# Optimization experiments

Measured on AMD Instinct MI355X. Metric: run time of the kernel, lower is better.

Reference implementation:

```python
import jax, jax.numpy as jnp
import numpy as np

B, H, S, D = 2, 16, 2048, 128


def setup_inputs() -> dict:
    key = jax.random.key(0)
    kq, kk, kv, km = jax.random.split(key, 4)
    Q = jax.random.normal(kq, (B, H, S, D), dtype=jnp.float32)
    K = jax.random.normal(kk, (B, H, S, D), dtype=jnp.float32)
    V = jax.random.normal(kv, (B, H, S, D), dtype=jnp.float32)
    mask = jax.random.randint(km, (B, 1, S, S), 0, 2, dtype=jnp.int32)
    scale = jnp.float32(1.0 / np.sqrt(D))
    return {"Q": Q, "K": K, "V": V, "mask": mask, "scale": scale}


def reference(Q, K, V, mask, scale):
    # attention scores: [B, H, Sq, Sk]
    attention = jnp.einsum('bhqd,bhkd->bhqk', Q, K) * scale
    NEG_BIG = jnp.float32(-1e9)
    attention = jnp.where(mask == 0, NEG_BIG, attention)
    attention = jax.nn.softmax(attention, axis=-1)
    # context: [B, H, Sq, Dv]
    context = jnp.einsum('bhqk,bhkd->bhqd', attention, V)
    return (context, attention)
```

## Files before the change

kernel.cpp:

```cpp
#include <hip/hip_runtime.h>

#define Bb 2
#define Hh 16
#define Ss 2048
#define Dd 128
#define NWrd (Ss / 64)
#define NBLK (Bb * Hh * (Ss / 64))

typedef _Float16 half_t;
typedef __attribute__((ext_vector_type(4))) float floatx4;
typedef __attribute__((ext_vector_type(8))) _Float16 halfx8;
typedef unsigned long long u64;

__global__ __launch_bounds__(256) void cvt_qk_kernel(
    const float* __restrict__ Q, const float* __restrict__ K,
    const float* __restrict__ scale_p,
    half_t* __restrict__ Qh, half_t* __restrict__ Kh) {
  const float s = scale_p[0];
  size_t i = ((size_t)blockIdx.x * 256 + threadIdx.x) * 8;
  floatx4 a0 = *(const floatx4*)(Q + i);
  floatx4 a1 = *(const floatx4*)(Q + i + 4);
  halfx8 hq = {(half_t)(a0.x * s), (half_t)(a0.y * s), (half_t)(a0.z * s),
               (half_t)(a0.w * s), (half_t)(a1.x * s), (half_t)(a1.y * s),
               (half_t)(a1.z * s), (half_t)(a1.w * s)};
  *(halfx8*)(Qh + i) = hq;
  floatx4 b0 = *(const floatx4*)(K + i);
  floatx4 b1 = *(const floatx4*)(K + i + 4);
  halfx8 hk = {(half_t)b0.x, (half_t)b0.y, (half_t)b0.z, (half_t)b0.w,
               (half_t)b1.x, (half_t)b1.y, (half_t)b1.z, (half_t)b1.w};
  *(halfx8*)(Kh + i) = hk;
}

__global__ __launch_bounds__(256) void vt_kernel(const float* __restrict__ V,
                                                 half_t* __restrict__ Vt) {
  __shared__ __align__(16) half_t t[64 * 72];
  const int bh = blockIdx.z;
  const int k0 = blockIdx.x * 64;
  const int d0 = blockIdx.y * 64;
  const int tid = threadIdx.x;
  const float* src = V + ((size_t)bh * Ss + k0) * Dd + d0;
  for (int idx = tid; idx < 64 * 16; idx += 256) {
    int r = idx >> 4;
    int c4 = (idx & 15) << 2;
    floatx4 v = *(const floatx4*)(src + (size_t)r * Dd + c4);
    t[(c4 + 0) * 72 + r] = (half_t)v.x;
    t[(c4 + 1) * 72 + r] = (half_t)v.y;
    t[(c4 + 2) * 72 + r] = (half_t)v.z;
    t[(c4 + 3) * 72 + r] = (half_t)v.w;
  }
  __syncthreads();
  half_t* dst = Vt + ((size_t)bh * Dd + d0) * Ss + k0;
  for (int idx = tid; idx < 64 * 8; idx += 256) {
    int r = idx >> 3;
    int c8 = (idx & 7) << 3;
    *(halfx8*)(dst + (size_t)r * Ss + c8) = *(const halfx8*)&t[r * 72 + c8];
  }
}

__global__ __launch_bounds__(256) void mask_pack_kernel(
    const int* __restrict__ mask, u64* __restrict__ mb) {
  size_t w = (size_t)blockIdx.x * 4 + (threadIdx.x >> 6);
  int lane = threadIdx.x & 63;
  int m = mask[w * 64 + lane];
  u64 bal = __ballot(m != 0);
  if (lane == 0) mb[w] = bal;
}

__global__ __launch_bounds__(256, 4) void attn_kernel(
    const half_t* __restrict__ Qh, const half_t* __restrict__ Kh,
    const u64* __restrict__ Mb, const half_t* __restrict__ Vt,
    float* __restrict__ ctx_out, float* __restrict__ attn_out) {
  __shared__ __align__(16) half_t Ks[64 * 136];
  __shared__ __align__(16) half_t Ps[4 * 16 * 72];

  const int tid = threadIdx.x;
  const int wave = tid >> 6;
  const int lane = tid & 63;
  const int quad = lane >> 4;
  const int l16 = lane & 15;

  const int wg = blockIdx.x + 32 * (blockIdx.y + Hh * blockIdx.z);
  const int v = (wg & 7) * (NBLK / 8) + (wg >> 3);
  const int q0 = (v & 31) * 64;
  const int bh = v >> 5;
  const int bidx = bh >> 4;

  const half_t* Qg = Qh + ((size_t)bh * Ss + q0) * Dd;
  const half_t* Kg = Kh + (size_t)bh * Ss * Dd;
  const half_t* Vtg = Vt + (size_t)bh * Dd * Ss;
  const u64* Mg = Mb + ((size_t)bidx * Ss + q0) * NWrd;

  const int arow = 16 * wave + l16;
  halfx8 qa[4];
#pragma unroll
  for (int ks = 0; ks < 4; ++ks)
    qa[ks] = *(const halfx8*)(Qg + (size_t)arow * Dd + ks * 32 + quad * 8);

  const int lrow = 16 * wave + quad * 4;
  const int qrow = q0 + lrow;
  const u64* Mrow = Mg + (size_t)lrow * NWrd;
  float lacc[4] = {0.f, 0.f, 0.f, 0.f};

  const int s_r = tid >> 4;
  const int s_c = (tid & 15) << 3;

  halfx8 kpre[4];
#pragma unroll
  for (int it = 0; it < 4; ++it)
    kpre[it] = *(const halfx8*)(Kg + (size_t)(s_r + it * 16) * Dd + s_c);

  for (int kt = 0; kt < NWrd; ++kt) {
    const int k0 = kt * 64;
    __syncthreads();
#pragma unroll
    for (int it = 0; it < 4; ++it)
      *(halfx8*)&Ks[(s_r + it * 16) * 136 + s_c] = kpre[it];
    if (kt + 1 < NWrd) {
#pragma unroll
      for (int it = 0; it < 4; ++it)
        kpre[it] = *(const halfx8*)(Kg + (size_t)(k0 + 64 + s_r + it * 16) * Dd + s_c);
    }
    u64 mw[4];
#pragma unroll
    for (int r = 0; r < 4; ++r) mw[r] = Mrow[(size_t)r * NWrd + kt];
    __syncthreads();
#pragma unroll
    for (int nt = 0; nt < 4; ++nt) {
      floatx4 acc = {0.f, 0.f, 0.f, 0.f};
#pragma unroll
      for (int ks = 0; ks < 4; ++ks) {
        halfx8 bf = *(const halfx8*)&Ks[(nt * 16 + l16) * 136 + ks * 32 + quad * 8];
        acc = __builtin_amdgcn_mfma_f32_16x16x32_f16(qa[ks], bf, acc, 0, 0, 0);
      }
      const int sh = nt * 16 + l16;
#pragma unroll
      for (int r = 0; r < 4; ++r) {
        float e = ((mw[r] >> sh) & 1) ? __expf(acc[r]) : 0.0f;
        lacc[r] += e;
      }
    }
  }
  float inv[4];
#pragma unroll
  for (int r = 0; r < 4; ++r) {
    float s = lacc[r];
    s += __shfl_xor(s, 1);
    s += __shfl_xor(s, 2);
    s += __shfl_xor(s, 4);
    s += __shfl_xor(s, 8);
    inv[r] = 1.0f / s;
  }

  floatx4 cacc[8];
#pragma unroll
  for (int i = 0; i < 8; ++i) cacc[i] = (floatx4){0.f, 0.f, 0.f, 0.f};
  float* attn_row = attn_out + (size_t)bh * Ss * Ss + (size_t)qrow * Ss;

#pragma unroll
  for (int it = 0; it < 4; ++it)
    kpre[it] = *(const halfx8*)(Kg + (size_t)(s_r + it * 16) * Dd + s_c);

  for (int kt = 0; kt < NWrd; ++kt) {
    const int k0 = kt * 64;
    __syncthreads();
#pragma unroll
    for (int it = 0; it < 4; ++it)
      *(halfx8*)&Ks[(s_r + it * 16) * 136 + s_c] = kpre[it];
    if (kt + 1 < NWrd) {
#pragma unroll
      for (int it = 0; it < 4; ++it)
        kpre[it] = *(const halfx8*)(Kg + (size_t)(k0 + 64 + s_r + it * 16) * Dd + s_c);
    }
    u64 mw[4];
#pragma unroll
    for (int r = 0; r < 4; ++r) mw[r] = Mrow[(size_t)r * NWrd + kt];
    __syncthreads();
#pragma unroll
    for (int nt = 0; nt < 4; ++nt) {
      floatx4 acc = {0.f, 0.f, 0.f, 0.f};
#pragma unroll
      for (int ks = 0; ks < 4; ++ks) {
        halfx8 bf = *(const halfx8*)&Ks[(nt * 16 + l16) * 136 + ks * 32 + quad * 8];
        acc = __builtin_amdgcn_mfma_f32_16x16x32_f16(qa[ks], bf, acc, 0, 0, 0);
      }
      const int sh = nt * 16 + l16;
#pragma unroll
      for (int r = 0; r < 4; ++r) {
        float p = ((mw[r] >> sh) & 1) ? __expf(acc[r]) * inv[r] : 0.0f;
        __builtin_nontemporal_store(p, &attn_row[(size_t)r * Ss + k0 + sh]);
        Ps[wave * (16 * 72) + (quad * 4 + r) * 72 + sh] = (half_t)p;
      }
    }
    halfx8 pa0 = *(const halfx8*)&Ps[wave * (16 * 72) + l16 * 72 + quad * 8];
    halfx8 pa1 = *(const halfx8*)&Ps[wave * (16 * 72) + l16 * 72 + 32 + quad * 8];
#pragma unroll
    for (int nt2 = 0; nt2 < 8; ++nt2) {
      const half_t* vrow = Vtg + (size_t)(nt2 * 16 + l16) * Ss + k0 + quad * 8;
      halfx8 bv0 = *(const halfx8*)(vrow);
      cacc[nt2] = __builtin_amdgcn_mfma_f32_16x16x32_f16(pa0, bv0, cacc[nt2], 0, 0, 0);
      halfx8 bv1 = *(const halfx8*)(vrow + 32);
      cacc[nt2] = __builtin_amdgcn_mfma_f32_16x16x32_f16(pa1, bv1, cacc[nt2], 0, 0, 0);
    }
  }

  float* ctx = ctx_out + (size_t)bh * Ss * Dd;
#pragma unroll
  for (int nt2 = 0; nt2 < 8; ++nt2) {
#pragma unroll
    for (int r = 0; r < 4; ++r) {
      ctx[(size_t)(qrow + r) * Dd + nt2 * 16 + l16] = cacc[nt2][r];
    }
  }
}

extern "C" void kernel_launch(void* const* d_in, const int* in_sizes, int n_in,
                              void* d_out, int out_size, void* d_ws, size_t ws_size,
                              hipStream_t stream) {
  const float* Q = (const float*)d_in[0];
  const float* K = (const float*)d_in[1];
  const float* V = (const float*)d_in[2];
  const int* mask = (const int*)d_in[3];
  const float* scale = (const float*)d_in[4];
  float* ctx = (float*)d_out;
  float* attn = (float*)d_out + (size_t)Bb * Hh * Ss * Dd;

  const size_t nqk = (size_t)Bb * Hh * Ss * Dd;
  half_t* Qh = (half_t*)d_ws;
  half_t* Kh = Qh + nqk;
  half_t* Vt = Kh + nqk;
  u64* Mbits = (u64*)(Vt + nqk);

  cvt_qk_kernel<<<nqk / (256 * 8), 256, 0, stream>>>(Q, K, scale, Qh, Kh);
  dim3 gt(Ss / 64, Dd / 64, Bb * Hh);
  vt_kernel<<<gt, 256, 0, stream>>>(V, Vt);
  mask_pack_kernel<<<((size_t)Bb * Ss * NWrd) / 4, 256, 0, stream>>>(mask, Mbits);
  dim3 gm(Ss / 64, Hh, Bb);
  attn_kernel<<<gm, 256, 0, stream>>>(Qh, Kh, Mbits, Vt, ctx, attn);
}
```

Before: 887.2 us.

## Read K fragments directly from global memory and fold log2e into Q scale

Removes the shared-memory K tile, its register prefetch and both block-wide barriers per key tile. Each wave now loads its K MFMA operands straight from global memory and relies on the cache for reuse across the four waves. Q is prescaled by log2(e), so the softmax uses exp2f instead of __expf. An explicit lgkmcnt wait is added before reading back the per-wave P tile, which would otherwise rely on the barrier that was removed. The risk is more global/L2 traffic and latency for K, since the four waves now fetch the same K rows redundantly.

```diff
diff --git a/kernel.cpp b/kernel.cpp
--- a/kernel.cpp
+++ b/kernel.cpp
@@ -16,7 +16,7 @@
     const float* __restrict__ Q, const float* __restrict__ K,
     const float* __restrict__ scale_p,
     half_t* __restrict__ Qh, half_t* __restrict__ Kh) {
-  const float s = scale_p[0];
+  const float s = scale_p[0] * 1.4426950408889634f;
   size_t i = ((size_t)blockIdx.x * 256 + threadIdx.x) * 8;
   floatx4 a0 = *(const floatx4*)(Q + i);
   floatx4 a1 = *(const floatx4*)(Q + i + 4);
@@ -70,7 +70,6 @@
     const half_t* __restrict__ Qh, const half_t* __restrict__ Kh,
     const u64* __restrict__ Mb, const half_t* __restrict__ Vt,
     float* __restrict__ ctx_out, float* __restrict__ attn_out) {
-  __shared__ __align__(16) half_t Ks[64 * 136];
   __shared__ __align__(16) half_t Ps[4 * 16 * 72];
 
   const int tid = threadIdx.x;
@@ -101,41 +100,24 @@
   const u64* Mrow = Mg + (size_t)lrow * NWrd;
   float lacc[4] = {0.f, 0.f, 0.f, 0.f};
 
-  const int s_r = tid >> 4;
-  const int s_c = (tid & 15) << 3;
-
-  halfx8 kpre[4];
-#pragma unroll
-  for (int it = 0; it < 4; ++it)
-    kpre[it] = *(const halfx8*)(Kg + (size_t)(s_r + it * 16) * Dd + s_c);
-
   for (int kt = 0; kt < NWrd; ++kt) {
     const int k0 = kt * 64;
-    __syncthreads();
-#pragma unroll
-    for (int it = 0; it < 4; ++it)
-      *(halfx8*)&Ks[(s_r + it * 16) * 136 + s_c] = kpre[it];
-    if (kt + 1 < NWrd) {
-#pragma unroll
-      for (int it = 0; it < 4; ++it)
-        kpre[it] = *(const halfx8*)(Kg + (size_t)(k0 + 64 + s_r + it * 16) * Dd + s_c);
-    }
     u64 mw[4];
 #pragma unroll
     for (int r = 0; r < 4; ++r) mw[r] = Mrow[(size_t)r * NWrd + kt];
-    __syncthreads();
 #pragma unroll
     for (int nt = 0; nt < 4; ++nt) {
+      const half_t* krow = Kg + (size_t)(k0 + nt * 16 + l16) * Dd + quad * 8;
       floatx4 acc = {0.f, 0.f, 0.f, 0.f};
 #pragma unroll
       for (int ks = 0; ks < 4; ++ks) {
-        halfx8 bf = *(const halfx8*)&Ks[(nt * 16 + l16) * 136 + ks * 32 + quad * 8];
+        halfx8 bf = *(const halfx8*)(krow + ks * 32);
         acc = __builtin_amdgcn_mfma_f32_16x16x32_f16(qa[ks], bf, acc, 0, 0, 0);
       }
       const int sh = nt * 16 + l16;
 #pragma unroll
       for (int r = 0; r < 4; ++r) {
-        float e = ((mw[r] >> sh) & 1) ? __expf(acc[r]) : 0.0f;
+        float e = ((mw[r] >> sh) & 1) ? exp2f(acc[r]) : 0.0f;
         lacc[r] += e;
       }
     }
@@ -156,41 +138,29 @@
   for (int i = 0; i < 8; ++i) cacc[i] = (floatx4){0.f, 0.f, 0.f, 0.f};
   float* attn_row = attn_out + (size_t)bh * Ss * Ss + (size_t)qrow * Ss;
 
-#pragma unroll
-  for (int it = 0; it < 4; ++it)
-    kpre[it] = *(const halfx8*)(Kg + (size_t)(s_r + it * 16) * Dd + s_c);
-
   for (int kt = 0; kt < NWrd; ++kt) {
     const int k0 = kt * 64;
-    __syncthreads();
-#pragma unroll
-    for (int it = 0; it < 4; ++it)
-      *(halfx8*)&Ks[(s_r + it * 16) * 136 + s_c] = kpre[it];
-    if (kt + 1 < NWrd) {
-#pragma unroll
-      for (int it = 0; it < 4; ++it)
-        kpre[it] = *(const halfx8*)(Kg + (size_t)(k0 + 64 + s_r + it * 16) * Dd + s_c);
-    }
     u64 mw[4];
 #pragma unroll
     for (int r = 0; r < 4; ++r) mw[r] = Mrow[(size_t)r * NWrd + kt];
-    __syncthreads();
 #pragma unroll
     for (int nt = 0; nt < 4; ++nt) {
+      const half_t* krow = Kg + (size_t)(k0 + nt * 16 + l16) * Dd + quad * 8;
       floatx4 acc = {0.f, 0.f, 0.f, 0.f};
 #pragma unroll
       for (int ks = 0; ks < 4; ++ks) {
-        halfx8 bf = *(const halfx8*)&Ks[(nt * 16 + l16) * 136 + ks * 32 + quad * 8];
+        halfx8 bf = *(const halfx8*)(krow + ks * 32);
         acc = __builtin_amdgcn_mfma_f32_16x16x32_f16(qa[ks], bf, acc, 0, 0, 0);
       }
       const int sh = nt * 16 + l16;
 #pragma unroll
       for (int r = 0; r < 4; ++r) {
-        float p = ((mw[r] >> sh) & 1) ? __expf(acc[r]) * inv[r] : 0.0f;
+        float p = ((mw[r] >> sh) & 1) ? exp2f(acc[r]) * inv[r] : 0.0f;
         __builtin_nontemporal_store(p, &attn_row[(size_t)r * Ss + k0 + sh]);
         Ps[wave * (16 * 72) + (quad * 4 + r) * 72 + sh] = (half_t)p;
       }
     }
+    asm volatile("s_waitcnt lgkmcnt(0)" ::: "memory");
     halfx8 pa0 = *(const halfx8*)&Ps[wave * (16 * 72) + l16 * 72 + quad * 8];
     halfx8 pa1 = *(const halfx8*)&Ps[wave * (16 * 72) + l16 * 72 + 32 + quad * 8];
 #pragma unroll
```

After: 1.292 ms. 1.46x slower.

## Cache unnormalized fp16 probabilities in workspace instead of recomputing QK^T

Applied to the files above, without the earlier changes.

The first pass now writes the unnormalized exp scores as fp16 to a global workspace. The second pass reads them back, normalizes, stores the attention matrix, and multiplies by V staged through shared memory, so the second QK^T matmul is gone. The log2e factor is folded into the Q scale so exp2f can replace __expf. This swaps recompute for extra global traffic (an fp16 S×S write and read), and the old two-pass kernel is kept as a fallback when the workspace is too small.

```diff
diff --git a/kernel.cpp b/kernel.cpp
--- a/kernel.cpp
+++ b/kernel.cpp
@@ -16,7 +16,7 @@
     const float* __restrict__ Q, const float* __restrict__ K,
     const float* __restrict__ scale_p,
     half_t* __restrict__ Qh, half_t* __restrict__ Kh) {
-  const float s = scale_p[0];
+  const float s = scale_p[0] * 1.4426950408889634f;
   size_t i = ((size_t)blockIdx.x * 256 + threadIdx.x) * 8;
   floatx4 a0 = *(const floatx4*)(Q + i);
   floatx4 a1 = *(const floatx4*)(Q + i + 4);
@@ -66,12 +66,16 @@
   if (lane == 0) mb[w] = bal;
 }
 
-__global__ __launch_bounds__(256, 4) void attn_kernel(
+__global__ __launch_bounds__(256, 4) void attn_fused(
     const half_t* __restrict__ Qh, const half_t* __restrict__ Kh,
     const u64* __restrict__ Mb, const half_t* __restrict__ Vt,
-    float* __restrict__ ctx_out, float* __restrict__ attn_out) {
-  __shared__ __align__(16) half_t Ks[64 * 136];
-  __shared__ __align__(16) half_t Ps[4 * 16 * 72];
+    half_t* __restrict__ Pw, float* __restrict__ ctx_out,
+    float* __restrict__ attn_out) {
+  __shared__ __align__(16) half_t smem[64 * 136 + 4 * 16 * 72];
+  __shared__ float invs[64];
+  half_t* Ks = smem;
+  half_t* Ps = smem + 64 * 136;
+  half_t* Vts = smem;
 
   const int tid = threadIdx.x;
   const int wave = tid >> 6;
@@ -89,6 +93,7 @@
   const half_t* Kg = Kh + (size_t)bh * Ss * Dd;
   const half_t* Vtg = Vt + (size_t)bh * Dd * Ss;
   const u64* Mg = Mb + ((size_t)bidx * Ss + q0) * NWrd;
+  half_t* Pwg = Pw + ((size_t)bh * Ss + q0) * Ss;
 
   const int arow = 16 * wave + l16;
   halfx8 qa[4];
@@ -101,6 +106,8 @@
   const u64* Mrow = Mg + (size_t)lrow * NWrd;
   float lacc[4] = {0.f, 0.f, 0.f, 0.f};
 
+  half_t* Pl = Pwg + (size_t)arow * Ss + quad * 8;
+
   const int s_r = tid >> 4;
   const int s_c = (tid & 15) << 3;
 
@@ -135,11 +142,18 @@
       const int sh = nt * 16 + l16;
 #pragma unroll
       for (int r = 0; r < 4; ++r) {
-        float e = ((mw[r] >> sh) & 1) ? __expf(acc[r]) : 0.0f;
+        float e = ((mw[r] >> sh) & 1) ? exp2f(acc[r]) : 0.0f;
         lacc[r] += e;
-      }
-    }
-  }
+        Ps[wave * (16 * 72) + (quad * 4 + r) * 72 + sh] = (half_t)e;
+      }
+    }
+    asm volatile("s_waitcnt lgkmcnt(0)" ::: "memory");
+    halfx8 pa0 = *(const halfx8*)&Ps[wave * (16 * 72) + l16 * 72 + quad * 8];
+    halfx8 pa1 = *(const halfx8*)&Ps[wave * (16 * 72) + l16 * 72 + 32 + quad * 8];
+    *(halfx8*)(Pl + k0) = pa0;
+    *(halfx8*)(Pl + k0 + 32) = pa1;
+  }
+
   float inv[4];
 #pragma unroll
   for (int r = 0; r < 4; ++r) {
@@ -150,12 +164,117 @@
     s += __shfl_xor(s, 8);
     inv[r] = 1.0f / s;
   }
+#pragma unroll
+  for (int r = 0; r < 4; ++r) invs[wave * 16 + quad * 4 + r] = inv[r];
+  __syncthreads();
+  const float invf = invs[wave * 16 + l16];
 
   floatx4 cacc[8];
 #pragma unroll
   for (int i = 0; i < 8; ++i) cacc[i] = (floatx4){0.f, 0.f, 0.f, 0.f};
-  float* attn_row = attn_out + (size_t)bh * Ss * Ss + (size_t)qrow * Ss;
-
+  float* arow_p = attn_out + ((size_t)bh * Ss + q0 + arow) * Ss + quad * 8;
+
+  const int v_r = tid >> 3;
+  const int v_c = (tid & 7) << 3;
+  halfx8 vpre[4];
+#pragma unroll
+  for (int it = 0; it < 4; ++it)
+    vpre[it] = *(const halfx8*)(Vtg + (size_t)(v_r + it * 32) * Ss + v_c);
+
+  for (int kt = 0; kt < NWrd; ++kt) {
+    const int k0 = kt * 64;
+    __syncthreads();
+#pragma unroll
+    for (int it = 0; it < 4; ++it)
+      *(halfx8*)&Vts[(v_r + it * 32) * 72 + v_c] = vpre[it];
+    if (kt + 1 < NWrd) {
+#pragma unroll
+      for (int it = 0; it < 4; ++it)
+        vpre[it] = *(const halfx8*)(Vtg + (size_t)(v_r + it * 32) * Ss + k0 + 64 + v_c);
+    }
+    halfx8 pa0 = *(const halfx8*)(Pl + k0);
+    halfx8 pa1 = *(const halfx8*)(Pl + k0 + 32);
+    __syncthreads();
+
+    floatx4 f0a, f0b, f1a, f1b;
+    halfx8 ph0, ph1;
+#pragma unroll
+    for (int j = 0; j < 4; ++j) {
+      f0a[j] = (float)pa0[j] * invf;
+      f0b[j] = (float)pa0[j + 4] * invf;
+      f1a[j] = (float)pa1[j] * invf;
+      f1b[j] = (float)pa1[j + 4] * invf;
+    }
+#pragma unroll
+    for (int j = 0; j < 4; ++j) {
+      ph0[j] = (half_t)f0a[j];
+      ph0[j + 4] = (half_t)f0b[j];
+      ph1[j] = (half_t)f1a[j];
+      ph1[j + 4] = (half_t)f1b[j];
+    }
+    __builtin_nontemporal_store(f0a, (floatx4*)(arow_p + k0));
+    __builtin_nontemporal_store(f0b, (floatx4*)(arow_p + k0 + 4));
+    __builtin_nontemporal_store(f1a, (floatx4*)(arow_p + k0 + 32));
+    __builtin_nontemporal_store(f1b, (floatx4*)(arow_p + k0 + 36));
+
+#pragma unroll
+    for (int nt2 = 0; nt2 < 8; ++nt2) {
+      halfx8 bv0 = *(const halfx8*)&Vts[(nt2 * 16 + l16) * 72 + quad * 8];
+      cacc[nt2] = __builtin_amdgcn_mfma_f32_16x16x32_f16(ph0, bv0, cacc[nt2], 0, 0, 0);
+      halfx8 bv1 = *(const halfx8*)&Vts[(nt2 * 16 + l16) * 72 + 32 + quad * 8];
+      cacc[nt2] = __builtin_amdgcn_mfma_f32_16x16x32_f16(ph1, bv1, cacc[nt2], 0, 0, 0);
+    }
+  }
+
+  float* ctx = ctx_out + (size_t)bh * Ss * Dd;
+#pragma unroll
+  for (int nt2 = 0; nt2 < 8; ++nt2) {
+#pragma unroll
+    for (int r = 0; r < 4; ++r) {
+      ctx[(size_t)(qrow + r) * Dd + nt2 * 16 + l16] = cacc[nt2][r];
+    }
+  }
+}
+
+__global__ __launch_bounds__(256, 4) void attn_2pass(
+    const half_t* __restrict__ Qh, const half_t* __restrict__ Kh,
+    const u64* __restrict__ Mb, const half_t* __restrict__ Vt,
+    float* __restrict__ ctx_out, float* __restrict__ attn_out) {
+  __shared__ __align__(16) half_t Ks[64 * 136];
+  __shared__ __align__(16) half_t Ps[4 * 16 * 72];
+
+  const int tid = threadIdx.x;
+  const int wave = tid >> 6;
+  const int lane = tid & 63;
+  const int quad = lane >> 4;
+  const int l16 = lane & 15;
+
+  const int wg = blockIdx.x + 32 * (blockIdx.y + Hh * blockIdx.z);
+  const int v = (wg & 7) * (NBLK / 8) + (wg >> 3);
+  const int q0 = (v & 31) * 64;
+  const int bh = v >> 5;
+  const int bidx = bh >> 4;
+
+  const half_t* Qg = Qh + ((size_t)bh * Ss + q0) * Dd;
+  const half_t* Kg = Kh + (size_t)bh * Ss * Dd;
+  const half_t* Vtg = Vt + (size_t)bh * Dd * Ss;
+  const u64* Mg = Mb + ((size_t)bidx * Ss + q0) * NWrd;
+
+  const int arow = 16 * wave + l16;
+  halfx8 qa[4];
+#pragma unroll
+  for (int ks = 0; ks < 4; ++ks)
+    qa[ks] = *(const halfx8*)(Qg + (size_t)arow * Dd + ks * 32 + quad * 8);
+
+  const int lrow = 16 * wave + quad * 4;
+  const int qrow = q0 + lrow;
+  const u64* Mrow = Mg + (size_t)lrow * NWrd;
+  float lacc[4] = {0.f, 0.f, 0.f, 0.f};
+
+  const int s_r = tid >> 4;
+  const int s_c = (tid & 15) << 3;
+
+  halfx8 kpre[4];
 #pragma unroll
   for (int it = 0; it < 4; ++it)
     kpre[it] = *(const halfx8*)(Kg + (size_t)(s_r + it * 16) * Dd + s_c);
@@ -186,11 +305,63 @@
       const int sh = nt * 16 + l16;
 #pragma unroll
       for (int r = 0; r < 4; ++r) {
-        float p = ((mw[r] >> sh) & 1) ? __expf(acc[r]) * inv[r] : 0.0f;
+        float e = ((mw[r] >> sh) & 1) ? exp2f(acc[r]) : 0.0f;
+        lacc[r] += e;
+      }
+    }
+  }
+  float inv[4];
+#pragma unroll
+  for (int r = 0; r < 4; ++r) {
+    float s = lacc[r];
+    s += __shfl_xor(s, 1);
+    s += __shfl_xor(s, 2);
+    s += __shfl_xor(s, 4);
+    s += __shfl_xor(s, 8);
+    inv[r] = 1.0f / s;
+  }
+
+  floatx4 cacc[8];
+#pragma unroll
+  for (int i = 0; i < 8; ++i) cacc[i] = (floatx4){0.f, 0.f, 0.f, 0.f};
+  float* attn_row = attn_out + (size_t)bh * Ss * Ss + (size_t)qrow * Ss;
+
+#pragma unroll
+  for (int it = 0; it < 4; ++it)
+    kpre[it] = *(const halfx8*)(Kg + (size_t)(s_r + it * 16) * Dd + s_c);
+
+  for (int kt = 0; kt < NWrd; ++kt) {
+    const int k0 = kt * 64;
+    __syncthreads();
+#pragma unroll
+    for (int it = 0; it < 4; ++it)
+      *(halfx8*)&Ks[(s_r + it * 16) * 136 + s_c] = kpre[it];
+    if (kt + 1 < NWrd) {
+#pragma unroll
+      for (int it = 0; it < 4; ++it)
+        kpre[it] = *(const halfx8*)(Kg + (size_t)(k0 + 64 + s_r + it * 16) * Dd + s_c);
+    }
+    u64 mw[4];
+#pragma unroll
+    for (int r = 0; r < 4; ++r) mw[r] = Mrow[(size_t)r * NWrd + kt];
+    __syncthreads();
+#pragma unroll
+    for (int nt = 0; nt < 4; ++nt) {
+      floatx4 acc = {0.f, 0.f, 0.f, 0.f};
+#pragma unroll
+      for (int ks = 0; ks < 4; ++ks) {
+        halfx8 bf = *(const halfx8*)&Ks[(nt * 16 + l16) * 136 + ks * 32 + quad * 8];
+        acc = __builtin_amdgcn_mfma_f32_16x16x32_f16(qa[ks], bf, acc, 0, 0, 0);
+      }
+      const int sh = nt * 16 + l16;
+#pragma unroll
+      for (int r = 0; r < 4; ++r) {
+        float p = ((mw[r] >> sh) & 1) ? exp2f(acc[r]) * inv[r] : 0.0f;
         __builtin_nontemporal_store(p, &attn_row[(size_t)r * Ss + k0 + sh]);
         Ps[wave * (16 * 72) + (quad * 4 + r) * 72 + sh] = (half_t)p;
       }
     }
+    asm volatile("s_waitcnt lgkmcnt(0)" ::: "memory");
     halfx8 pa0 = *(const halfx8*)&Ps[wave * (16 * 72) + l16 * 72 + quad * 8];
     halfx8 pa1 = *(const halfx8*)&Ps[wave * (16 * 72) + l16 * 72 + 32 + quad * 8];
 #pragma unroll
@@ -225,15 +396,25 @@
   float* attn = (float*)d_out + (size_t)Bb * Hh * Ss * Dd;
 
   const size_t nqk = (size_t)Bb * Hh * Ss * Dd;
+  const size_t nmask = (size_t)Bb * Ss * NWrd;
+  const size_t npw = (size_t)Bb * Hh * Ss * Ss;
   half_t* Qh = (half_t*)d_ws;
   half_t* Kh = Qh + nqk;
   half_t* Vt = Kh + nqk;
   u64* Mbits = (u64*)(Vt + nqk);
+  half_t* Pw = (half_t*)(Mbits + nmask);
+
+  const size_t need = 3 * nqk * sizeof(half_t) + nmask * sizeof(u64) +
+                      npw * sizeof(half_t);
 
   cvt_qk_kernel<<<nqk / (256 * 8), 256, 0, stream>>>(Q, K, scale, Qh, Kh);
   dim3 gt(Ss / 64, Dd / 64, Bb * Hh);
   vt_kernel<<<gt, 256, 0, stream>>>(V, Vt);
-  mask_pack_kernel<<<((size_t)Bb * Ss * NWrd) / 4, 256, 0, stream>>>(mask, Mbits);
+  mask_pack_kernel<<<(nmask) / 4, 256, 0, stream>>>(mask, Mbits);
   dim3 gm(Ss / 64, Hh, Bb);
-  attn_kernel<<<gm, 256, 0, stream>>>(Qh, Kh, Mbits, Vt, ctx, attn);
-}
+  if (ws_size >= need) {
+    attn_fused<<<gm, 256, 0, stream>>>(Qh, Kh, Mbits, Vt, Pw, ctx, attn);
+  } else {
+    attn_2pass<<<gm, 256, 0, stream>>>(Qh, Kh, Mbits, Vt, ctx, attn);
+  }
+}
```

Result: no change. 874.9 us (-1.4%).
